# Kernel tuning notes

Measured on AMD Instinct MI355X. Metric: run time of the kernel, lower is better.

The kernel has to match this reference:

```python
import jax, jax.numpy as jnp
import numpy as np

DICT_SIZE = 200000
EMBED_DIM = 128
NUM_NEG = 5
BATCH = 131072


def setup_inputs() -> dict:
    key = jax.random.key(0)
    k1, k2, k3, k4, k5 = jax.random.split(key, 5)
    return {
        "second_emb": jax.random.normal(k1, (DICT_SIZE, EMBED_DIM), dtype=jnp.float32) * 0.1,
        "context_emb": jax.random.normal(k2, (DICT_SIZE, EMBED_DIM), dtype=jnp.float32) * 0.1,
        "v_i": jax.random.randint(k3, (BATCH,), 0, DICT_SIZE),
        "v_j": jax.random.randint(k4, (BATCH,), 0, DICT_SIZE),
        "negsamples": jax.random.randint(k5, (NUM_NEG, BATCH), 0, DICT_SIZE),
    }


def reference(second_emb, context_emb, v_i, v_j, negsamples):
    # order == 'second':
    # v_i one-hot @ second_embeddings  == row gather from second table
    # v_j / negatives one-hot @ context_embeddings == row gather from context table
    vi_e = second_emb[v_i]          # [B, E]
    vj_e = context_emb[v_j]         # [B, E]
    neg_e = context_emb[negsamples]  # [K, B, E]

    pos = jax.nn.log_sigmoid(jnp.sum(vi_e * vj_e, axis=1))          # [B]
    neg_scores = jnp.einsum("be,kbe->kb", vi_e, neg_e)               # [K, B]
    neg = jnp.sum(jax.nn.log_sigmoid(-neg_scores), axis=0)           # [B]

    loss = pos + neg
    return -jnp.mean(loss)
```

## Files before the change

kernel.cpp:

```cpp
#include <hip/hip_runtime.h>
#include <hip/hip_bf16.h>

#define EDIM 128
#define KNEG 5

__global__ __launch_bounds__(256) void sgns_loss_kernel(
    const float* __restrict__ second_emb,
    const float* __restrict__ context_emb,
    const int* __restrict__ v_i,
    const int* __restrict__ v_j,
    const int* __restrict__ negs,
    float* __restrict__ out,
    int B)
{
    const int tid   = blockIdx.x * blockDim.x + threadIdx.x;
    const int lane  = threadIdx.x & 63;
    const int half  = lane >> 5;
    const int sub   = lane & 31;
    const int gwave = tid >> 6;
    const int nwaves = (gridDim.x * blockDim.x) >> 6;

    float acc = 0.0f;

    for (int base = gwave * 4; base < B; base += nwaves * 4) {
        const int b0 = base + half * 2;
        const int b1 = b0 + 1;

        const int i0  = v_i[b0];
        const int i1  = v_i[b1];
        const int j0  = v_j[b0];
        const int j1  = v_j[b1];
        const int n00 = negs[0 * B + b0];
        const int n01 = negs[1 * B + b0];
        const int n02 = negs[2 * B + b0];
        const int n03 = negs[3 * B + b0];
        const int n04 = negs[4 * B + b0];
        const int n10 = negs[0 * B + b1];
        const int n11 = negs[1 * B + b1];
        const int n12 = negs[2 * B + b1];
        const int n13 = negs[3 * B + b1];
        const int n14 = negs[4 * B + b1];

        const float4 a0  = ((const float4*)(second_emb  + (size_t)i0  * EDIM))[sub];
        const float4 a1  = ((const float4*)(second_emb  + (size_t)i1  * EDIM))[sub];
        const float4 p0  = ((const float4*)(context_emb + (size_t)j0  * EDIM))[sub];
        const float4 p1  = ((const float4*)(context_emb + (size_t)j1  * EDIM))[sub];
        const float4 q00 = ((const float4*)(context_emb + (size_t)n00 * EDIM))[sub];
        const float4 q01 = ((const float4*)(context_emb + (size_t)n01 * EDIM))[sub];
        const float4 q02 = ((const float4*)(context_emb + (size_t)n02 * EDIM))[sub];
        const float4 q03 = ((const float4*)(context_emb + (size_t)n03 * EDIM))[sub];
        const float4 q04 = ((const float4*)(context_emb + (size_t)n04 * EDIM))[sub];
        const float4 q10 = ((const float4*)(context_emb + (size_t)n10 * EDIM))[sub];
        const float4 q11 = ((const float4*)(context_emb + (size_t)n11 * EDIM))[sub];
        const float4 q12 = ((const float4*)(context_emb + (size_t)n12 * EDIM))[sub];
        const float4 q13 = ((const float4*)(context_emb + (size_t)n13 * EDIM))[sub];
        const float4 q14 = ((const float4*)(context_emb + (size_t)n14 * EDIM))[sub];

        float d[12];
        d[0]  = a0.x * p0.x  + a0.y * p0.y  + a0.z * p0.z  + a0.w * p0.w;
        d[1]  = a0.x * q00.x + a0.y * q00.y + a0.z * q00.z + a0.w * q00.w;
        d[2]  = a0.x * q01.x + a0.y * q01.y + a0.z * q01.z + a0.w * q01.w;
        d[3]  = a0.x * q02.x + a0.y * q02.y + a0.z * q02.z + a0.w * q02.w;
        d[4]  = a0.x * q03.x + a0.y * q03.y + a0.z * q03.z + a0.w * q03.w;
        d[5]  = a0.x * q04.x + a0.y * q04.y + a0.z * q04.z + a0.w * q04.w;
        d[6]  = a1.x * p1.x  + a1.y * p1.y  + a1.z * p1.z  + a1.w * p1.w;
        d[7]  = a1.x * q10.x + a1.y * q10.y + a1.z * q10.z + a1.w * q10.w;
        d[8]  = a1.x * q11.x + a1.y * q11.y + a1.z * q11.z + a1.w * q11.w;
        d[9]  = a1.x * q12.x + a1.y * q12.y + a1.z * q12.z + a1.w * q12.w;
        d[10] = a1.x * q13.x + a1.y * q13.y + a1.z * q13.z + a1.w * q13.w;
        d[11] = a1.x * q14.x + a1.y * q14.y + a1.z * q14.z + a1.w * q14.w;

        #pragma unroll
        for (int off = 1; off <= 16; off <<= 1) {
            #pragma unroll
            for (int m = 0; m < 12; ++m)
                d[m] += __shfl_xor(d[m], off);
        }

        float x = 0.0f;
        bool active = false;
        if (sub < 6) {
            x = (sub == 0) ? d[0] : -d[sub];
            active = true;
        } else if (sub >= 8 && sub < 14) {
            const int s = sub - 8;
            x = (s == 0) ? d[6] : -d[6 + s];
            active = true;
        }
        if (active) {
            acc += fminf(x, 0.0f) - log1pf(expf(-fabsf(x)));
        }
    }

    #pragma unroll
    for (int off = 32; off >= 1; off >>= 1)
        acc += __shfl_xor(acc, off);

    __shared__ float wsum[4];
    const int wid = threadIdx.x >> 6;
    if ((threadIdx.x & 63) == 0) wsum[wid] = acc;
    __syncthreads();

    if (threadIdx.x == 0) {
        float s = wsum[0] + wsum[1] + wsum[2] + wsum[3];
        atomicAdd(out, s * (-1.0f / (float)B));
    }
}

extern "C" void kernel_launch(void* const* d_in, const int* in_sizes, int n_in,
                              void* d_out, int out_size, void* d_ws, size_t ws_size,
                              hipStream_t stream) {
    const float* second_emb  = (const float*)d_in[0];
    const float* context_emb = (const float*)d_in[1];
    const int*   v_i  = (const int*)d_in[2];
    const int*   v_j  = (const int*)d_in[3];
    const int*   negs = (const int*)d_in[4];
    float* out = (float*)d_out;
    const int B = in_sizes[2];

    hipMemsetAsync(d_out, 0, sizeof(float), stream);

    dim3 block(256);
    dim3 grid(2048);
    sgns_loss_kernel<<<grid, block, 0, stream>>>(
        second_emb, context_emb, v_i, v_j, negs, out, B);
}
```

Before: 240.1 us.

## Restructure SGNS gather to full-wave row loads with prefetched vector indices

Each wave now handles four batch rows, and every lane loads a float2 slice of each 128-float row, replacing the half-wave float4 layout. Indices are read as int4 vectors from a wave-uniform base and prefetched one iteration ahead, so gathers are not stalled on index loads. Dot products are reduced with a paired shuffle tree that packs two sums per lane, and the logsigmoid uses fast __expf/__logf. Every lane computes the logsigmoid redundantly, and the sum is rescaled by 1/32 to compensate. This trades more log/exp work and register pressure for fewer index loads and more gathers in flight per wave.

```diff
diff --git a/kernel.cpp b/kernel.cpp
--- a/kernel.cpp
+++ b/kernel.cpp
@@ -1,8 +1,10 @@
 #include <hip/hip_runtime.h>
-#include <hip/hip_bf16.h>
 
 #define EDIM 128
-#define KNEG 5
+
+__device__ __forceinline__ float fast_logsig(float x) {
+    return fminf(x, 0.0f) - __logf(1.0f + __expf(-fabsf(x)));
+}
 
 __global__ __launch_bounds__(256) void sgns_loss_kernel(
     const float* __restrict__ second_emb,
@@ -13,84 +15,129 @@
     float* __restrict__ out,
     int B)
 {
-    const int tid   = blockIdx.x * blockDim.x + threadIdx.x;
-    const int lane  = threadIdx.x & 63;
-    const int half  = lane >> 5;
-    const int sub   = lane & 31;
-    const int gwave = tid >> 6;
+    const int tid    = blockIdx.x * blockDim.x + threadIdx.x;
+    const int lane   = threadIdx.x & 63;
+    const int gwave  = tid >> 6;
     const int nwaves = (gridDim.x * blockDim.x) >> 6;
+    const int step   = nwaves * 4;
+
+    const float2* __restrict__ se2 = (const float2*)second_emb;
+    const float2* __restrict__ ce2 = (const float2*)context_emb;
 
     float acc = 0.0f;
 
-    for (int base = gwave * 4; base < B; base += nwaves * 4) {
-        const int b0 = base + half * 2;
-        const int b1 = b0 + 1;
+    int base = gwave * 4;
 
-        const int i0  = v_i[b0];
-        const int i1  = v_i[b1];
-        const int j0  = v_j[b0];
-        const int j1  = v_j[b1];
-        const int n00 = negs[0 * B + b0];
-        const int n01 = negs[1 * B + b0];
-        const int n02 = negs[2 * B + b0];
-        const int n03 = negs[3 * B + b0];
-        const int n04 = negs[4 * B + b0];
-        const int n10 = negs[0 * B + b1];
-        const int n11 = negs[1 * B + b1];
-        const int n12 = negs[2 * B + b1];
-        const int n13 = negs[3 * B + b1];
-        const int n14 = negs[4 * B + b1];
+#define LOAD_IDX(BB, VI, VJ, N0, N1, N2, N3, N4) do {            \
+        const int ub_ = __builtin_amdgcn_readfirstlane(BB);      \
+        VI = *(const int4*)(v_i + ub_);                          \
+        VJ = *(const int4*)(v_j + ub_);                          \
+        N0 = *(const int4*)(negs + 0 * (size_t)B + ub_);         \
+        N1 = *(const int4*)(negs + 1 * (size_t)B + ub_);         \
+        N2 = *(const int4*)(negs + 2 * (size_t)B + ub_);         \
+        N3 = *(const int4*)(negs + 3 * (size_t)B + ub_);         \
+        N4 = *(const int4*)(negs + 4 * (size_t)B + ub_);         \
+    } while (0)
 
-        const float4 a0  = ((const float4*)(second_emb  + (size_t)i0  * EDIM))[sub];
-        const float4 a1  = ((const float4*)(second_emb  + (size_t)i1  * EDIM))[sub];
-        const float4 p0  = ((const float4*)(context_emb + (size_t)j0  * EDIM))[sub];
-        const float4 p1  = ((const float4*)(context_emb + (size_t)j1  * EDIM))[sub];
-        const float4 q00 = ((const float4*)(context_emb + (size_t)n00 * EDIM))[sub];
-        const float4 q01 = ((const float4*)(context_emb + (size_t)n01 * EDIM))[sub];
-        const float4 q02 = ((const float4*)(context_emb + (size_t)n02 * EDIM))[sub];
-        const float4 q03 = ((const float4*)(context_emb + (size_t)n03 * EDIM))[sub];
-        const float4 q04 = ((const float4*)(context_emb + (size_t)n04 * EDIM))[sub];
-        const float4 q10 = ((const float4*)(context_emb + (size_t)n10 * EDIM))[sub];
-        const float4 q11 = ((const float4*)(context_emb + (size_t)n11 * EDIM))[sub];
-        const float4 q12 = ((const float4*)(context_emb + (size_t)n12 * EDIM))[sub];
-        const float4 q13 = ((const float4*)(context_emb + (size_t)n13 * EDIM))[sub];
-        const float4 q14 = ((const float4*)(context_emb + (size_t)n14 * EDIM))[sub];
+#define ROW(TBL, IDX) (TBL)[(((size_t)(uint32_t)(IDX)) << 6) + lane]
 
-        float d[12];
-        d[0]  = a0.x * p0.x  + a0.y * p0.y  + a0.z * p0.z  + a0.w * p0.w;
-        d[1]  = a0.x * q00.x + a0.y * q00.y + a0.z * q00.z + a0.w * q00.w;
-        d[2]  = a0.x * q01.x + a0.y * q01.y + a0.z * q01.z + a0.w * q01.w;
-        d[3]  = a0.x * q02.x + a0.y * q02.y + a0.z * q02.z + a0.w * q02.w;
-        d[4]  = a0.x * q03.x + a0.y * q03.y + a0.z * q03.z + a0.w * q03.w;
-        d[5]  = a0.x * q04.x + a0.y * q04.y + a0.z * q04.z + a0.w * q04.w;
-        d[6]  = a1.x * p1.x  + a1.y * p1.y  + a1.z * p1.z  + a1.w * p1.w;
-        d[7]  = a1.x * q10.x + a1.y * q10.y + a1.z * q10.z + a1.w * q10.w;
-        d[8]  = a1.x * q11.x + a1.y * q11.y + a1.z * q11.z + a1.w * q11.w;
-        d[9]  = a1.x * q12.x + a1.y * q12.y + a1.z * q12.z + a1.w * q12.w;
-        d[10] = a1.x * q13.x + a1.y * q13.y + a1.z * q13.z + a1.w * q13.w;
-        d[11] = a1.x * q14.x + a1.y * q14.y + a1.z * q14.z + a1.w * q14.w;
+    if (base < B) {
+        int4 cvi, cvj, cn0, cn1, cn2, cn3, cn4;
+        LOAD_IDX(base, cvi, cvj, cn0, cn1, cn2, cn3, cn4);
 
-        #pragma unroll
-        for (int off = 1; off <= 16; off <<= 1) {
+        for (;;) {
+            const float2 a0  = ROW(se2, cvi.x);
+            const float2 p0  = ROW(ce2, cvj.x);
+            const float2 q00 = ROW(ce2, cn0.x);
+            const float2 q01 = ROW(ce2, cn1.x);
+            const float2 q02 = ROW(ce2, cn2.x);
+            const float2 q03 = ROW(ce2, cn3.x);
+            const float2 q04 = ROW(ce2, cn4.x);
+            const float2 a1  = ROW(se2, cvi.y);
+            const float2 p1  = ROW(ce2, cvj.y);
+            const float2 q10 = ROW(ce2, cn0.y);
+            const float2 q11 = ROW(ce2, cn1.y);
+            const float2 q12 = ROW(ce2, cn2.y);
+            const float2 q13 = ROW(ce2, cn3.y);
+            const float2 q14 = ROW(ce2, cn4.y);
+            const float2 a2  = ROW(se2, cvi.z);
+            const float2 p2  = ROW(ce2, cvj.z);
+            const float2 q20 = ROW(ce2, cn0.z);
+            const float2 q21 = ROW(ce2, cn1.z);
+            const float2 q22 = ROW(ce2, cn2.z);
+            const float2 q23 = ROW(ce2, cn3.z);
+            const float2 q24 = ROW(ce2, cn4.z);
+            const float2 a3  = ROW(se2, cvi.w);
+            const float2 p3  = ROW(ce2, cvj.w);
+            const float2 q30 = ROW(ce2, cn0.w);
+            const float2 q31 = ROW(ce2, cn1.w);
+            const float2 q32 = ROW(ce2, cn2.w);
+            const float2 q33 = ROW(ce2, cn3.w);
+            const float2 q34 = ROW(ce2, cn4.w);
+
+            const int  nb   = base + step;
+            const bool more = (nb < B);
+            int4 nvi = cvi, nvj = cvj, nn0 = cn0, nn1 = cn1,
+                 nn2 = cn2, nn3 = cn3, nn4 = cn4;
+            if (more) LOAD_IDX(nb, nvi, nvj, nn0, nn1, nn2, nn3, nn4);
+
+            float d[24];
+            d[0]  = a0.x*p0.x  + a0.y*p0.y;
+            d[1]  = a0.x*q00.x + a0.y*q00.y;
+            d[2]  = a0.x*q01.x + a0.y*q01.y;
+            d[3]  = a0.x*q02.x + a0.y*q02.y;
+            d[4]  = a0.x*q03.x + a0.y*q03.y;
+            d[5]  = a0.x*q04.x + a0.y*q04.y;
+            d[6]  = a1.x*p1.x  + a1.y*p1.y;
+            d[7]  = a1.x*q10.x + a1.y*q10.y;
+            d[8]  = a1.x*q11.x + a1.y*q11.y;
+            d[9]  = a1.x*q12.x + a1.y*q12.y;
+            d[10] = a1.x*q13.x + a1.y*q13.y;
+            d[11] = a1.x*q14.x + a1.y*q14.y;
+            d[12] = a2.x*p2.x  + a2.y*p2.y;
+            d[13] = a2.x*q20.x + a2.y*q20.y;
+            d[14] = a2.x*q21.x + a2.y*q21.y;
+            d[15] = a2.x*q22.x + a2.y*q22.y;
+            d[16] = a2.x*q23.x + a2.y*q23.y;
+            d[17] = a2.x*q24.x + a2.y*q24.y;
+            d[18] = a3.x*p3.x  + a3.y*p3.y;
+            d[19] = a3.x*q30.x + a3.y*q30.y;
+            d[20] = a3.x*q31.x + a3.y*q31.y;
+            d[21] = a3.x*q32.x + a3.y*q32.y;
+            d[22] = a3.x*q33.x + a3.y*q33.y;
+            d[23] = a3.x*q34.x + a3.y*q34.y;
+
+            float r[12];
             #pragma unroll
-            for (int m = 0; m < 12; ++m)
-                d[m] += __shfl_xor(d[m], off);
-        }
+            for (int m = 0; m < 12; ++m) {
+                const float e0 = d[2*m]     + __shfl_xor(d[2*m],     1);
+                const float e1 = d[2*m + 1] + __shfl_xor(d[2*m + 1], 1);
+                float mm = (lane & 1) ? e1 : e0;
+                mm += __shfl_xor(mm, 2);
+                mm += __shfl_xor(mm, 4);
+                mm += __shfl_xor(mm, 8);
+                mm += __shfl_xor(mm, 16);
+                mm += __shfl_xor(mm, 32);
+                r[m] = mm;
+            }
 
-        float x = 0.0f;
-        bool active = false;
-        if (sub < 6) {
-            x = (sub == 0) ? d[0] : -d[sub];
-            active = true;
-        } else if (sub >= 8 && sub < 14) {
-            const int s = sub - 8;
-            x = (s == 0) ? d[6] : -d[6 + s];
-            active = true;
-        }
-        if (active) {
-            acc += fminf(x, 0.0f) - log1pf(expf(-fabsf(x)));
+            const bool odd = (lane & 1) != 0;
+            #pragma unroll
+            for (int m = 0; m < 12; ++m) {
+                const float v = r[m];
+                const float x = ((m % 3) == 0) ? (odd ? -v : v) : -v;
+                acc += fast_logsig(x);
+            }
+
+            if (!more) break;
+            base = nb;
+            cvi = nvi; cvj = nvj;
+            cn0 = nn0; cn1 = nn1; cn2 = nn2; cn3 = nn3; cn4 = nn4;
         }
     }
+
+#undef ROW
+#undef LOAD_IDX
 
     #pragma unroll
     for (int off = 32; off >= 1; off >>= 1)
@@ -102,8 +149,8 @@
     __syncthreads();
 
     if (threadIdx.x == 0) {
-        float s = wsum[0] + wsum[1] + wsum[2] + wsum[3];
-        atomicAdd(out, s * (-1.0f / (float)B));
+        const float s = wsum[0] + wsum[1] + wsum[2] + wsum[3];
+        atomicAdd(out, s * (-1.0f / (32.0f * (float)B)));
     }
 }
 
```

Result: slower. 246.0 us (+2.5%).

## Prefetch next iteration's indices via wave-uniform int4 loads and use fast logsigmoid

Applied to the files above, without the earlier changes.

Index loads become wave-uniform int4 loads (readfirstlane base), so the compiler can issue scalar loads, and the next iteration's indices are fetched before the current dot products are computed. This software pipelining is meant to hide the dependent index-then-row latency chain. log1pf/expf are replaced with the __logf/__expf intrinsics, trading a little accuracy for fewer instructions. Row addressing uses 32-bit unsigned shifts. The int4 loads assume B is divisible by 4 and that the index arrays are 16-byte aligned.

```diff
diff --git a/kernel.cpp b/kernel.cpp
--- a/kernel.cpp
+++ b/kernel.cpp
@@ -1,8 +1,10 @@
 #include <hip/hip_runtime.h>
-#include <hip/hip_bf16.h>
 
 #define EDIM 128
-#define KNEG 5
+
+__device__ __forceinline__ float fast_logsig(float x) {
+    return fminf(x, 0.0f) - __logf(1.0f + __expf(-fabsf(x)));
+}
 
 __global__ __launch_bounds__(256) void sgns_loss_kernel(
     const float* __restrict__ second_emb,
@@ -13,84 +15,116 @@
     float* __restrict__ out,
     int B)
 {
-    const int tid   = blockIdx.x * blockDim.x + threadIdx.x;
-    const int lane  = threadIdx.x & 63;
-    const int half  = lane >> 5;
-    const int sub   = lane & 31;
-    const int gwave = tid >> 6;
+    const int tid    = blockIdx.x * blockDim.x + threadIdx.x;
+    const int lane   = threadIdx.x & 63;
+    const int half   = lane >> 5;
+    const int sub    = lane & 31;
+    const int gwave  = tid >> 6;
     const int nwaves = (gridDim.x * blockDim.x) >> 6;
+    const int step   = nwaves * 4;
+
+    const float4* __restrict__ A = (const float4*)second_emb;
+    const float4* __restrict__ C = (const float4*)context_emb;
 
     float acc = 0.0f;
 
-    for (int base = gwave * 4; base < B; base += nwaves * 4) {
-        const int b0 = base + half * 2;
-        const int b1 = b0 + 1;
+#define LOAD_IDX(BB, VI, VJ, N0, N1, N2, N3, N4) do {            \
+        const int ub_ = __builtin_amdgcn_readfirstlane(BB);      \
+        VI = *(const int4*)(v_i + ub_);                          \
+        VJ = *(const int4*)(v_j + ub_);                          \
+        N0 = *(const int4*)(negs + 0 * (size_t)B + ub_);         \
+        N1 = *(const int4*)(negs + 1 * (size_t)B + ub_);         \
+        N2 = *(const int4*)(negs + 2 * (size_t)B + ub_);         \
+        N3 = *(const int4*)(negs + 3 * (size_t)B + ub_);         \
+        N4 = *(const int4*)(negs + 4 * (size_t)B + ub_);         \
+    } while (0)
 
-        const int i0  = v_i[b0];
-        const int i1  = v_i[b1];
-        const int j0  = v_j[b0];
-        const int j1  = v_j[b1];
-        const int n00 = negs[0 * B + b0];
-        const int n01 = negs[1 * B + b0];
-        const int n02 = negs[2 * B + b0];
-        const int n03 = negs[3 * B + b0];
-        const int n04 = negs[4 * B + b0];
-        const int n10 = negs[0 * B + b1];
-        const int n11 = negs[1 * B + b1];
-        const int n12 = negs[2 * B + b1];
-        const int n13 = negs[3 * B + b1];
-        const int n14 = negs[4 * B + b1];
+#define ROW(TBL, IDX) (TBL)[(((size_t)(uint32_t)(IDX)) << 5) + sub]
 
-        const float4 a0  = ((const float4*)(second_emb  + (size_t)i0  * EDIM))[sub];
-        const float4 a1  = ((const float4*)(second_emb  + (size_t)i1  * EDIM))[sub];
-        const float4 p0  = ((const float4*)(context_emb + (size_t)j0  * EDIM))[sub];
-        const float4 p1  = ((const float4*)(context_emb + (size_t)j1  * EDIM))[sub];
-        const float4 q00 = ((const float4*)(context_emb + (size_t)n00 * EDIM))[sub];
-        const float4 q01 = ((const float4*)(context_emb + (size_t)n01 * EDIM))[sub];
-        const float4 q02 = ((const float4*)(context_emb + (size_t)n02 * EDIM))[sub];
-        const float4 q03 = ((const float4*)(context_emb + (size_t)n03 * EDIM))[sub];
-        const float4 q04 = ((const float4*)(context_emb + (size_t)n04 * EDIM))[sub];
-        const float4 q10 = ((const float4*)(context_emb + (size_t)n10 * EDIM))[sub];
-        const float4 q11 = ((const float4*)(context_emb + (size_t)n11 * EDIM))[sub];
-        const float4 q12 = ((const float4*)(context_emb + (size_t)n12 * EDIM))[sub];
-        const float4 q13 = ((const float4*)(context_emb + (size_t)n13 * EDIM))[sub];
-        const float4 q14 = ((const float4*)(context_emb + (size_t)n14 * EDIM))[sub];
+    int base = gwave * 4;
+    if (base < B) {
+        int4 cvi, cvj, cn0, cn1, cn2, cn3, cn4;
+        LOAD_IDX(base, cvi, cvj, cn0, cn1, cn2, cn3, cn4);
 
-        float d[12];
-        d[0]  = a0.x * p0.x  + a0.y * p0.y  + a0.z * p0.z  + a0.w * p0.w;
-        d[1]  = a0.x * q00.x + a0.y * q00.y + a0.z * q00.z + a0.w * q00.w;
-        d[2]  = a0.x * q01.x + a0.y * q01.y + a0.z * q01.z + a0.w * q01.w;
-        d[3]  = a0.x * q02.x + a0.y * q02.y + a0.z * q02.z + a0.w * q02.w;
-        d[4]  = a0.x * q03.x + a0.y * q03.y + a0.z * q03.z + a0.w * q03.w;
-        d[5]  = a0.x * q04.x + a0.y * q04.y + a0.z * q04.z + a0.w * q04.w;
-        d[6]  = a1.x * p1.x  + a1.y * p1.y  + a1.z * p1.z  + a1.w * p1.w;
-        d[7]  = a1.x * q10.x + a1.y * q10.y + a1.z * q10.z + a1.w * q10.w;
-        d[8]  = a1.x * q11.x + a1.y * q11.y + a1.z * q11.z + a1.w * q11.w;
-        d[9]  = a1.x * q12.x + a1.y * q12.y + a1.z * q12.z + a1.w * q12.w;
-        d[10] = a1.x * q13.x + a1.y * q13.y + a1.z * q13.z + a1.w * q13.w;
-        d[11] = a1.x * q14.x + a1.y * q14.y + a1.z * q14.z + a1.w * q14.w;
+        for (;;) {
+            const int i0  = half ? cvi.z : cvi.x;
+            const int i1  = half ? cvi.w : cvi.y;
+            const int j0  = half ? cvj.z : cvj.x;
+            const int j1  = half ? cvj.w : cvj.y;
+            const int n00 = half ? cn0.z : cn0.x;
+            const int n01 = half ? cn1.z : cn1.x;
+            const int n02 = half ? cn2.z : cn2.x;
+            const int n03 = half ? cn3.z : cn3.x;
+            const int n04 = half ? cn4.z : cn4.x;
+            const int n10 = half ? cn0.w : cn0.y;
+            const int n11 = half ? cn1.w : cn1.y;
+            const int n12 = half ? cn2.w : cn2.y;
+            const int n13 = half ? cn3.w : cn3.y;
+            const int n14 = half ? cn4.w : cn4.y;
 
-        #pragma unroll
-        for (int off = 1; off <= 16; off <<= 1) {
+            const float4 a0  = ROW(A, i0);
+            const float4 p0  = ROW(C, j0);
+            const float4 q00 = ROW(C, n00);
+            const float4 q01 = ROW(C, n01);
+            const float4 q02 = ROW(C, n02);
+            const float4 q03 = ROW(C, n03);
+            const float4 q04 = ROW(C, n04);
+            const float4 a1  = ROW(A, i1);
+            const float4 p1  = ROW(C, j1);
+            const float4 q10 = ROW(C, n10);
+            const float4 q11 = ROW(C, n11);
+            const float4 q12 = ROW(C, n12);
+            const float4 q13 = ROW(C, n13);
+            const float4 q14 = ROW(C, n14);
+
+            const int  nb   = base + step;
+            const bool more = (nb < B);
+            int4 nvi = cvi, nvj = cvj, nn0 = cn0, nn1 = cn1,
+                 nn2 = cn2, nn3 = cn3, nn4 = cn4;
+            if (more) LOAD_IDX(nb, nvi, nvj, nn0, nn1, nn2, nn3, nn4);
+
+            float d[12];
+            d[0]  = a0.x * p0.x  + a0.y * p0.y  + a0.z * p0.z  + a0.w * p0.w;
+            d[1]  = a0.x * q00.x + a0.y * q00.y + a0.z * q00.z + a0.w * q00.w;
+            d[2]  = a0.x * q01.x + a0.y * q01.y + a0.z * q01.z + a0.w * q01.w;
+            d[3]  = a0.x * q02.x + a0.y * q02.y + a0.z * q02.z + a0.w * q02.w;
+            d[4]  = a0.x * q03.x + a0.y * q03.y + a0.z * q03.z + a0.w * q03.w;
+            d[5]  = a0.x * q04.x + a0.y * q04.y + a0.z * q04.z + a0.w * q04.w;
+            d[6]  = a1.x * p1.x  + a1.y * p1.y  + a1.z * p1.z  + a1.w * p1.w;
+            d[7]  = a1.x * q10.x + a1.y * q10.y + a1.z * q10.z + a1.w * q10.w;
+            d[8]  = a1.x * q11.x + a1.y * q11.y + a1.z * q11.z + a1.w * q11.w;
+            d[9]  = a1.x * q12.x + a1.y * q12.y + a1.z * q12.z + a1.w * q12.w;
+            d[10] = a1.x * q13.x + a1.y * q13.y + a1.z * q13.z + a1.w * q13.w;
+            d[11] = a1.x * q14.x + a1.y * q14.y + a1.z * q14.z + a1.w * q14.w;
+
             #pragma unroll
-            for (int m = 0; m < 12; ++m)
-                d[m] += __shfl_xor(d[m], off);
-        }
+            for (int off = 1; off <= 16; off <<= 1) {
+                #pragma unroll
+                for (int m = 0; m < 12; ++m)
+                    d[m] += __shfl_xor(d[m], off);
+            }
 
-        float x = 0.0f;
-        bool active = false;
-        if (sub < 6) {
-            x = (sub == 0) ? d[0] : -d[sub];
-            active = true;
-        } else if (sub >= 8 && sub < 14) {
-            const int s = sub - 8;
-            x = (s == 0) ? d[6] : -d[6 + s];
-            active = true;
-        }
-        if (active) {
-            acc += fminf(x, 0.0f) - log1pf(expf(-fabsf(x)));
+            float x = 0.0f;
+            bool active = false;
+            if (sub < 6) {
+                x = (sub == 0) ? d[0] : -d[sub];
+                active = true;
+            } else if (sub >= 8 && sub < 14) {
+                const int s = sub - 8;
+                x = (s == 0) ? d[6] : -d[6 + s];
+                active = true;
+            }
+            if (active) acc += fast_logsig(x);
+
+            if (!more) break;
+            base = nb;
+            cvi = nvi; cvj = nvj;
+            cn0 = nn0; cn1 = nn1; cn2 = nn2; cn3 = nn3; cn4 = nn4;
         }
     }
+
+#undef ROW
+#undef LOAD_IDX
 
     #pragma unroll
     for (int off = 32; off >= 1; off >>= 1)
@@ -102,7 +136,7 @@
     __syncthreads();
 
     if (threadIdx.x == 0) {
-        float s = wsum[0] + wsum[1] + wsum[2] + wsum[3];
+        const float s = wsum[0] + wsum[1] + wsum[2] + wsum[3];
         atomicAdd(out, s * (-1.0f / (float)B));
     }
 }
```

Result: no change. 241.7 us (+0.6%).
